# Kernel optimization log

Measured on AMD Instinct MI355X. Metric: run time of the kernel, lower is better.

Reference implementation:

```python
import jax, jax.numpy as jnp
import numpy as np
from jax import lax

D_MODEL = 2048
D_STATE = 16
D_CONV = 4
D_INNER = 4096   # expand * d_model
DT_RANK = 128    # ceil(d_model / 16)
BATCH = 4
SEQLEN = 2048


def setup_inputs() -> dict:
    key = jax.random.key(0)
    ks = jax.random.split(key, 8)
    rnd = lambda k, shape, s: jax.random.normal(k, shape, dtype=jnp.float32) * s
    hidden_states = rnd(ks[0], (BATCH, SEQLEN, D_MODEL), 1.0)
    in_proj_w = rnd(ks[1], (2 * D_INNER, D_MODEL), D_MODEL ** -0.5)
    conv_w = rnd(ks[2], (D_INNER, 1, D_CONV), 0.3)
    conv_b = rnd(ks[3], (D_INNER,), 0.1)
    x_proj_w = rnd(ks[4], (DT_RANK + 2 * D_STATE, D_INNER), D_INNER ** -0.5)
    dt_proj_w = rnd(ks[5], (D_INNER, DT_RANK), DT_RANK ** -0.5)
    dt_proj_b = rnd(ks[6], (D_INNER,), 0.5) - 2.0  # bias dt small, like mamba dt init
    out_proj_w = rnd(ks[7], (D_MODEL, D_INNER), D_INNER ** -0.5)
    # A init: -exp(log(arange(1..N))) broadcast over channels -> (d_state, d_inner)
    A = -jnp.tile(jnp.arange(1, D_STATE + 1, dtype=jnp.float32)[:, None], (1, D_INNER))
    D = jnp.ones((D_INNER,), dtype=jnp.float32)
    conv_state = jnp.zeros((BATCH, D_INNER, D_CONV), jnp.float32)
    ssm_state = jnp.zeros((BATCH, D_STATE, D_INNER), jnp.float32)
    last_token_ids = jnp.full((BATCH,), SEQLEN, dtype=jnp.int32)
    return dict(hidden_states=hidden_states, last_token_ids=last_token_ids,
                conv_state=conv_state, ssm_state=ssm_state,
                remove_padding=False, batch_size=BATCH,
                in_proj_w=in_proj_w, conv_w=conv_w, conv_b=conv_b,
                x_proj_w=x_proj_w, dt_proj_w=dt_proj_w, dt_proj_b=dt_proj_b,
                A=A, D=D, out_proj_w=out_proj_w)


def _mamba_forward(hidden_states, in_proj_w, conv_w, conv_b, x_proj_w,
                   dt_proj_w, dt_proj_b, A, D, out_proj_w):
    b, L, _ = hidden_states.shape
    # in_proj (no bias)
    xz = jnp.einsum('bld,ed->ble', hidden_states, in_proj_w)          # (b, L, 2*d_inner)
    x, z = jnp.split(xz, 2, axis=-1)
    x_bdl = x.transpose(0, 2, 1)                                       # (b, d_inner, L)
    # present conv state = last d_conv columns of pre-conv x (F.pad with negative pad)
    new_conv_state = x_bdl[:, :, L - D_CONV:]
    # causal depthwise conv1d (left pad d_conv-1 == pad-both then truncate to L)
    x_conv = lax.conv_general_dilated(
        x_bdl, conv_w, window_strides=(1,), padding=[(D_CONV - 1, 0)],
        feature_group_count=D_INNER,
        dimension_numbers=('NCH', 'OIH', 'NCH')) + conv_b[None, :, None]
    u = jax.nn.silu(x_conv).transpose(0, 2, 1)                          # (b, L, d_inner)
    # x_proj -> dt, B, C
    x_dbl = jnp.einsum('bld,ed->ble', u, x_proj_w)
    dt, Bm, Cm = jnp.split(x_dbl, [DT_RANK, DT_RANK + D_STATE], axis=-1)
    dt = jnp.einsum('blr,dr->bld', dt, dt_proj_w)                       # no bias here
    # selective scan (delta_bias=dt_proj_b, delta_softplus=True)
    delta = jax.nn.softplus(dt + dt_proj_b)                             # (b, L, d_inner)
    dBu = delta * u                                                     # (b, L, d_inner)

    def step(x_state, inp):
        d_i, bu_i, B_i, C_i = inp                                       # (b,d),(b,d),(b,n),(b,n)
        dA = jnp.exp(d_i[:, None, :] * A[None])                         # (b, n, d)
        x_state = dA * x_state + B_i[:, :, None] * bu_i[:, None, :]
        y = jnp.einsum('bnd,bn->bd', x_state, C_i)
        return x_state, y

    x0 = jnp.zeros((b, D_STATE, D_INNER), jnp.float32)
    xs = (delta.transpose(1, 0, 2), dBu.transpose(1, 0, 2),
          Bm.transpose(1, 0, 2), Cm.transpose(1, 0, 2))
    last_state, ys = lax.scan(step, x0, xs)
    y = ys.transpose(1, 0, 2) + u * D                                   # + D skip
    y = y * jax.nn.silu(z)                                              # gate
    out = jnp.einsum('bld,ed->ble', y, out_proj_w)                      # out_proj (no bias)
    return out, new_conv_state, last_state


def reference(hidden_states, last_token_ids, conv_state, ssm_state,
              remove_padding, batch_size,
              in_proj_w, conv_w, conv_b, x_proj_w, dt_proj_w, dt_proj_b,
              A, D, out_proj_w):
    # remove_padding=False and last_token_ids all == L: the torch per-sequence
    # loop is exactly one batched forward_impl with seqlen_offset=0.
    return _mamba_forward(hidden_states, in_proj_w, conv_w, conv_b, x_proj_w,
                          dt_proj_w, dt_proj_b, A, D, out_proj_w)
```

## Files before the change

kernel.cpp:

```cpp
#include <hip/hip_runtime.h>
#include <hip/hip_bf16.h>
#include <math.h>

typedef __attribute__((ext_vector_type(4))) float fvec4;
typedef __attribute__((ext_vector_type(2))) float fvec2;
typedef __attribute__((ext_vector_type(4))) int ivec4;
typedef __attribute__((ext_vector_type(4))) unsigned short usvec4;
typedef __attribute__((ext_vector_type(8))) short bf16x8;

#define SEQ 2048
#define DMODEL 2048
#define DINNER 4096
#define DSTATE 16
#define DTRANK 128
#define NB 4
#define MROWS (NB*SEQ)
#define NCHUNK 16
#define LC (SEQ/NCHUNK)

__device__ __forceinline__ float bf2f(unsigned short h){
  union{unsigned int u; float f;} v; v.u = ((unsigned int)h)<<16; return v.f;
}
__device__ __forceinline__ unsigned short f2bf(float f){
  union{float f; unsigned int u;} v; v.f=f;
  unsigned int r = v.u + 0x7fffu + ((v.u>>16)&1u);
  return (unsigned short)(r>>16);
}
__device__ __forceinline__ void async16(const void* g, void* l){
  __builtin_amdgcn_global_load_lds((const __attribute__((address_space(1))) void*)g,
                                   (__attribute__((address_space(3))) void*)l, 16, 0, 0);
}
__device__ __forceinline__ float sigf(float x){ return 1.f/(1.f+__expf(-x)); }

__global__ void cvt_bf16_kernel(const float* __restrict__ in, unsigned short* __restrict__ out, int n){
  int i = (blockIdx.x*256 + threadIdx.x)*4;
  if (i >= n) return;
  fvec4 v = *(const fvec4*)(in + i);
  usvec4 o;
  o[0]=f2bf(v[0]); o[1]=f2bf(v[1]); o[2]=f2bf(v[2]); o[3]=f2bf(v[3]);
  *(usvec4*)(out + i) = o;
}

template<int MODE>
__global__ __launch_bounds__(512, 2) void gemm256(
    const unsigned short* __restrict__ A,
    const unsigned short* __restrict__ B,
    int K, int nbx, int ldc,
    unsigned short* __restrict__ Cb1,
    unsigned short* __restrict__ Cb2,
    float* __restrict__ Cf)
{
  __shared__ __align__(16) unsigned short lds[65536];
  char* ldsc = (char*)lds;
  const int t = threadIdx.x;

  const int nwg = gridDim.x;
  const int cpx = nwg >> 3;
  const int bid = blockIdx.x;
  const int swzb = (bid & 7)*cpx + (bid >> 3);
  const int bx = swzb % nbx, by = swzb / nbx;

  const int bA0 = t*16, bA1 = 8192 + t*16;
  const int sw0 = bA0 ^ (((bA0>>7)&3)<<4);
  const int sw1 = bA1 ^ (((bA1>>7)&3)<<4);
  const int gr0 = sw0>>6, gc0 = (sw0&63)>>1;
  const int gr1 = sw1>>6, gc1 = (sw1&63)>>1;
  const unsigned short* Ab = A + (long)by*256*K;
  const unsigned short* Bb = B + (long)bx*256*K;
  const unsigned short* gA0 = Ab + (long)gr0*K + gc0;
  const unsigned short* gA1 = Ab + (long)gr1*K + gc1;
  const unsigned short* gB0 = Bb + (long)gr0*K + gc0;
  const unsigned short* gB1 = Bb + (long)gr1*K + gc1;

  const int wid = t>>6, lane = t&63;
  const int wm = wid>>2, wn = wid&3;
  const int fr = lane&15, fc = lane>>4;
  const int cb = (fc<<4) ^ (((fr>>1)&3)<<4);
  const int offA = (wm*128 + fr)*64 + cb;
  const int offB = 16384 + (wn*64 + fr)*64 + cb;

  fvec4 acc[8][4];
  #pragma unroll
  for (int i=0;i<8;i++){
    #pragma unroll
    for (int j=0;j<4;j++) acc[i][j] = (fvec4)(0.f);
  }

  const int NKT = K >> 5;
  auto stage = [&](int slot, int k0){
    char* sb = ldsc + slot*32768;
    async16(gA0 + k0, sb + t*16);
    async16(gA1 + k0, sb + 8192 + t*16);
    async16(gB0 + k0, sb + 16384 + t*16);
    async16(gB1 + k0, sb + 24576 + t*16);
  };

  stage(0, 0); stage(1, 32); stage(2, 64);

  for (int kt = 0; kt < NKT; ++kt){
    asm volatile("s_waitcnt vmcnt(8)" ::: "memory");
    __builtin_amdgcn_s_barrier();
    __builtin_amdgcn_sched_barrier(0);
    { int ks = kt + 3; if (ks > NKT-1) ks = NKT-1;
      stage((kt+3)&3, ks*32); }
    __builtin_amdgcn_sched_barrier(0);
    const char* sb = ldsc + (kt&3)*32768;
    bf16x8 af[8], bv[4];
    #pragma unroll
    for (int j=0;j<4;j++) bv[j] = *(const bf16x8*)(sb + offB + j*1024);
    #pragma unroll
    for (int i=0;i<8;i++) af[i] = *(const bf16x8*)(sb + offA + i*1024);
    __builtin_amdgcn_s_setprio(1);
    #pragma unroll
    for (int i=0;i<8;i++){
      #pragma unroll
      for (int j=0;j<4;j++){
        acc[i][j] = __builtin_amdgcn_mfma_f32_16x16x32_bf16(af[i], bv[j], acc[i][j], 0,0,0);
      }
    }
    __builtin_amdgcn_s_setprio(0);
  }

  const long crow0 = (long)by*256 + wm*128;
  const int  ccol0 = bx*256 + wn*64;
  #pragma unroll
  for (int i=0;i<8;i++){
    #pragma unroll
    for (int j=0;j<4;j++){
      #pragma unroll
      for (int q=0;q<4;q++){
        long rg = crow0 + i*16 + fc*4 + q;
        int  cg = ccol0 + j*16 + fr;
        float v = acc[i][j][q];
        if (MODE==0){
          if (cg < DINNER) Cb1[rg*DINNER + cg] = f2bf(v);
          else             Cb2[rg*DINNER + (cg-DINNER)] = f2bf(v);
        } else {
          Cf[rg*(long)ldc + cg] = v;
        }
      }
    }
  }
}

template<int MODE>
__global__ __launch_bounds__(256) void gemm_bt(
    const unsigned short* __restrict__ A,
    const unsigned short* __restrict__ B,
    int K, int Nreal,
    float* __restrict__ Cf,
    unsigned short* __restrict__ Cb1,
    const float* __restrict__ bias,
    int ldc)
{
  __shared__ __align__(16) unsigned short As[128*32];
  __shared__ __align__(16) unsigned short Bs[128*32];
  const int t = threadIdx.x;
  const int bx = blockIdx.x, by = blockIdx.y;
  const int wave = t>>6, lane = t&63;
  const int wr = (wave>>1)*64, wc = (wave&1)*64;
  const int fr = lane&15, fc = lane>>4;
  fvec4 acc[4][4];
  #pragma unroll
  for(int i=0;i<4;i++){
    #pragma unroll
    for(int j=0;j<4;j++){ acc[i][j] = (fvec4)(0.f); }
  }
  const int srow = t>>2;
  const int scol = (t&3)*8;
  long rowA = (long)by*128 + srow;
  int rB0 = bx*128 + srow;      if (rB0 > Nreal-1) rB0 = Nreal-1;
  int rB1 = bx*128 + 64 + srow; if (rB1 > Nreal-1) rB1 = Nreal-1;
  const unsigned short* gA0 = A + rowA*(long)K + scol;
  const unsigned short* gA1 = gA0 + 64L*K;
  const unsigned short* gB0 = B + (long)rB0*K + scol;
  const unsigned short* gB1 = B + (long)rB1*K + scol;
  unsigned short* lA0 = &As[t*8];
  unsigned short* lA1 = &As[2048 + t*8];
  unsigned short* lB0 = &Bs[t*8];
  unsigned short* lB1 = &Bs[2048 + t*8];

  for (int k0 = 0; k0 < K; k0 += 32){
    async16(gA0 + k0, lA0);
    async16(gA1 + k0, lA1);
    async16(gB0 + k0, lB0);
    async16(gB1 + k0, lB1);
    __syncthreads();
    bf16x8 af[4], bv[4];
    #pragma unroll
    for(int i=0;i<4;i++){
      af[i] = *(const bf16x8*)&As[(wr + i*16 + fr)*32 + fc*8];
      bv[i] = *(const bf16x8*)&Bs[(wc + i*16 + fr)*32 + fc*8];
    }
    #pragma unroll
    for(int i=0;i<4;i++){
      #pragma unroll
      for(int j=0;j<4;j++){
        acc[i][j] = __builtin_amdgcn_mfma_f32_16x16x32_bf16(af[i], bv[j], acc[i][j], 0,0,0);
      }
    }
    __syncthreads();
  }

  const long crow0 = (long)by*128 + wr;
  const int ccol0 = bx*128 + wc;
  #pragma unroll
  for(int i=0;i<4;i++){
    #pragma unroll
    for(int j=0;j<4;j++){
      #pragma unroll
      for(int q=0;q<4;q++){
        long rg = crow0 + i*16 + fc*4 + q;
        int  cg = ccol0 + j*16 + fr;
        float v = acc[i][j][q];
        if (MODE==1){
          if (cg < Nreal) Cf[rg*ldc + cg] = v;
        } else if (MODE==2){
          float x = v + bias[cg];
          float sp = (x > 20.f) ? x : log1pf(__expf(x));
          Cb1[rg*ldc + cg] = f2bf(sp);
        }
      }
    }
  }
}

__global__ __launch_bounds__(256) void conv_silu_kernel(
    const unsigned short* __restrict__ xb, const float* __restrict__ w,
    const float* __restrict__ bias, unsigned short* __restrict__ ub)
{
  int gid = blockIdx.x*256 + threadIdx.x;
  int d0 = (gid & 511)*8;
  long m = gid >> 9;
  int l = (int)(m & (SEQ-1));
  fvec4 w4[8];
  #pragma unroll
  for(int k=0;k<8;k++) w4[k] = *(const fvec4*)&w[(d0+k)*4];
  float acc[8];
  fvec4 b0 = *(const fvec4*)&bias[d0];
  fvec4 b1 = *(const fvec4*)&bias[d0+4];
  acc[0]=b0[0];acc[1]=b0[1];acc[2]=b0[2];acc[3]=b0[3];
  acc[4]=b1[0];acc[5]=b1[1];acc[6]=b1[2];acc[7]=b1[3];
  #pragma unroll
  for(int j=0;j<4;j++){
    int lj = l-3+j;
    if (lj >= 0){
      ivec4 xv = *(const ivec4*)&xb[(m-3+j)*DINNER + d0];
      float xs[8];
      #pragma unroll
      for(int q=0;q<4;q++){
        unsigned int wd = (unsigned int)xv[q];
        xs[2*q]   = bf2f((unsigned short)(wd & 0xffffu));
        xs[2*q+1] = bf2f((unsigned short)(wd >> 16));
      }
      #pragma unroll
      for(int k=0;k<8;k++) acc[k] += xs[k]*w4[k][j];
    }
  }
  ivec4 ov;
  #pragma unroll
  for(int q=0;q<4;q++){
    float y0 = acc[2*q]  * sigf(acc[2*q]);
    float y1 = acc[2*q+1]* sigf(acc[2*q+1]);
    ov[q] = (int)((unsigned)f2bf(y0) | ((unsigned)f2bf(y1) << 16));
  }
  *(ivec4*)&ub[m*DINNER + d0] = ov;
}

__global__ void conv_state_kernel(const unsigned short* __restrict__ xb, float* __restrict__ out){
  int i = blockIdx.x*256 + threadIdx.x;
  int b = i >> 14; int r = i & 16383; int dd = r >> 2; int j = r & 3;
  out[i] = bf2f(xb[((long)(b*SEQ + (SEQ-4) + j))*DINNER + dd]);
}

__global__ void cvt_dtr_kernel(const float* __restrict__ xdbl, unsigned short* __restrict__ dtr){
  int i = blockIdx.x*256 + threadIdx.x;
  long mrow = i >> 5; int c = (i & 31)*4;
  fvec4 v = *(const fvec4*)&xdbl[mrow*160 + c];
  usvec4 o; o[0]=f2bf(v[0]); o[1]=f2bf(v[1]); o[2]=f2bf(v[2]); o[3]=f2bf(v[3]);
  *(usvec4*)&dtr[mrow*DTRANK + c] = o;
}

__device__ __forceinline__ void exp_powers(float dl, float* e){
  float e1 = __expf(-dl);
  float p2 = e1*e1, p3 = p2*e1, p4 = p2*p2;
  float p5 = p4*e1, p6 = p4*p2, p7 = p4*p3, p8 = p4*p4;
  e[0]=e1; e[1]=p2; e[2]=p3; e[3]=p4; e[4]=p5; e[5]=p6; e[6]=p7; e[7]=p8;
  e[8]=p8*e1; e[9]=p8*p2; e[10]=p8*p3; e[11]=p8*p4;
  e[12]=p8*p5; e[13]=p8*p6; e[14]=p8*p7; e[15]=p8*p8;
}

__global__ __launch_bounds__(256) void scan_part1(
    const unsigned short* __restrict__ delta_b,
    const unsigned short* __restrict__ u_b,
    const float* __restrict__ xdbl,
    const float* __restrict__ Amat,
    float* __restrict__ S,
    float* __restrict__ sdelta)
{
  const int t = threadIdx.x;
  const int blk = blockIdx.x;
  const int c = blk & 15, b = (blk>>4)&3, d = (blk>>6)*256 + t;
  float a[16], s[16];
  #pragma unroll
  for (int n=0;n<16;n++){ a[n] = Amat[n*DINNER+d]; s[n]=0.f; }
  bool powA = true;
  #pragma unroll
  for (int n=0;n<16;n++) powA = powA && (a[n] == -(float)(n+1));
  float sd = 0.f;
  const long mbase = (long)b*SEQ + c*LC;

#define S1_BODY(EXPR_E) \
  for (int l=0;l<LC;l++){ \
    long m = mbase + l; \
    float dl = bf2f(delta_b[m*DINNER+d]); \
    float ul = bf2f(u_b[m*DINNER+d]); \
    const float* xb = &xdbl[m*160 + 128]; \
    float dbu = dl*ul; \
    sd += dl; \
    float e[16]; EXPR_E; \
    _Pragma("unroll") \
    for (int g=0; g<4; g++){ \
      fvec4 Bg = *(const fvec4*)(xb + 4*g); \
      _Pragma("unroll") \
      for (int q=0;q<4;q++){ \
        int n = g*4+q; \
        s[n] = e[n]*s[n] + Bg[q]*dbu; \
      } \
    } \
  }

  if (powA){
    S1_BODY(exp_powers(dl, e))
  } else {
    S1_BODY({ _Pragma("unroll") for (int n=0;n<16;n++) e[n] = __expf(dl*a[n]); })
  }
#undef S1_BODY

  const long base = ((long)(b*NCHUNK + c)*DSTATE)*DINNER + d;
  #pragma unroll
  for (int n=0;n<16;n++) S[base + (long)n*DINNER] = s[n];
  sdelta[(long)(b*NCHUNK+c)*DINNER + d] = sd;
}

__global__ __launch_bounds__(256) void scan_part2(
    const float* __restrict__ S,
    const float* __restrict__ sdelta,
    const float* __restrict__ Amat,
    float* __restrict__ Xin,
    float* __restrict__ last_state)
{
  int id = blockIdx.x*256 + threadIdx.x;
  int d = id & (DINNER-1);
  int n = (id>>12) & 15;
  int b = id>>16;
  float a = Amat[n*DINNER+d];
  float X = 0.f;
  #pragma unroll
  for (int c=0;c<NCHUNK;c++){
    long sb = ((long)(b*NCHUNK+c)*DSTATE + n)*DINNER + d;
    Xin[sb] = X;
    float sd = sdelta[(long)(b*NCHUNK+c)*DINNER + d];
    float Sc = S[sb];
    X = __expf(a*sd)*X + Sc;
  }
  last_state[((long)b*DSTATE + n)*DINNER + d] = X;
}

__global__ __launch_bounds__(256) void scan_part3(
    const unsigned short* __restrict__ delta_b,
    const unsigned short* __restrict__ u_b,
    const unsigned short* __restrict__ z_b,
    const float* __restrict__ xdbl,
    const float* __restrict__ Amat,
    const float* __restrict__ Dvec,
    const float* __restrict__ Xin,
    unsigned short* __restrict__ y_b)
{
  const int t = threadIdx.x;
  const int blk = blockIdx.x;
  const int c = blk & 15, b = (blk>>4)&3, d = (blk>>6)*256 + t;
  float a[16], s[16];
  const long xb0 = ((long)(b*NCHUNK + c)*DSTATE)*DINNER + d;
  #pragma unroll
  for (int n=0;n<16;n++){
    a[n] = Amat[n*DINNER+d];
    s[n] = Xin[xb0 + (long)n*DINNER];
  }
  bool powA = true;
  #pragma unroll
  for (int n=0;n<16;n++) powA = powA && (a[n] == -(float)(n+1));
  const float Dd = Dvec[d];
  const long mbase = (long)b*SEQ + c*LC;

#define S3_BODY(EXPR_E) \
  for (int l=0;l<LC;l++){ \
    long m = mbase + l; \
    float dl = bf2f(delta_b[m*DINNER+d]); \
    float ul = bf2f(u_b[m*DINNER+d]); \
    float zl = bf2f(z_b[m*DINNER+d]); \
    const float* xb = &xdbl[m*160 + 128]; \
    float dbu = dl*ul; \
    float y = 0.f; \
    float e[16]; EXPR_E; \
    _Pragma("unroll") \
    for (int g=0; g<4; g++){ \
      fvec4 Bg = *(const fvec4*)(xb + 4*g); \
      fvec4 Cg = *(const fvec4*)(xb + 16 + 4*g); \
      _Pragma("unroll") \
      for (int q=0;q<4;q++){ \
        int n = g*4+q; \
        s[n] = e[n]*s[n] + Bg[q]*dbu; \
        y += Cg[q]*s[n]; \
      } \
    } \
    float yy = y + ul*Dd; \
    float zs = zl*sigf(zl); \
    y_b[m*DINNER+d] = f2bf(yy*zs); \
  }

  if (powA){
    S3_BODY(exp_powers(dl, e))
  } else {
    S3_BODY({ _Pragma("unroll") for (int n=0;n<16;n++) e[n] = __expf(dl*a[n]); })
  }
#undef S3_BODY
}

extern "C" void kernel_launch(void* const* d_in, const int* in_sizes, int n_in,
                              void* d_out, int out_size, void* d_ws, size_t ws_size,
                              hipStream_t stream) {
  const float* hs     = (const float*)d_in[0];
  const float* w_in   = (const float*)d_in[6];
  const float* conv_w = (const float*)d_in[7];
  const float* conv_b = (const float*)d_in[8];
  const float* w_xp   = (const float*)d_in[9];
  const float* w_dt   = (const float*)d_in[10];
  const float* dt_bias= (const float*)d_in[11];
  const float* Amat   = (const float*)d_in[12];
  const float* Dvec   = (const float*)d_in[13];
  const float* w_out  = (const float*)d_in[14];
  float* out = (float*)d_out;

  char* ws = (char*)d_ws;
  const size_t MiB = (size_t)1 << 20;

  unsigned short *hs_b, *w_in_b, *x_b, *z_b, *u_b, *delta_b;
  unsigned short *wxp_b, *wdt_b, *wout_b, *dtr_b, *y_b;
  float *xdbl, *Sbuf, *Xin, *sdelta;

  if (ws_size >= 400*MiB){
    size_t off = 0;
    auto alloc = [&](size_t bytes)->void*{ void* p = ws + off; off += (bytes + 255) & ~(size_t)255; return p; };
    hs_b   = (unsigned short*)alloc((size_t)MROWS*DMODEL*2);
    w_in_b = (unsigned short*)alloc((size_t)2*DINNER*DMODEL*2);
    x_b    = (unsigned short*)alloc((size_t)MROWS*DINNER*2);
    z_b    = (unsigned short*)alloc((size_t)MROWS*DINNER*2);
    u_b    = (unsigned short*)alloc((size_t)MROWS*DINNER*2);
    delta_b= (unsigned short*)alloc((size_t)MROWS*DINNER*2);
    wxp_b  = (unsigned short*)alloc((size_t)160*DINNER*2);
    wdt_b  = (unsigned short*)alloc((size_t)DINNER*DTRANK*2);
    wout_b = (unsigned short*)alloc((size_t)DMODEL*DINNER*2);
    xdbl   = (float*)alloc((size_t)MROWS*160*4);
    dtr_b  = (unsigned short*)alloc((size_t)MROWS*DTRANK*2);
    Sbuf   = (float*)alloc((size_t)NB*NCHUNK*DSTATE*DINNER*4);
    Xin    = (float*)alloc((size_t)NB*NCHUNK*DSTATE*DINNER*4);
    sdelta = (float*)alloc((size_t)NB*NCHUNK*DINNER*4);
    y_b    = x_b;
  } else {
    hs_b    = (unsigned short*)(ws + 0);
    w_in_b  = (unsigned short*)(ws + 32*MiB);
    delta_b = (unsigned short*)(ws + 0);
    x_b     = (unsigned short*)(ws + 64*MiB);
    wxp_b   = (unsigned short*)(ws + 64*MiB);
    wdt_b   = (unsigned short*)(ws + 66*MiB);
    wout_b  = (unsigned short*)(ws + 68*MiB);
    xdbl    = (float*)         (ws + 84*MiB);
    dtr_b   = (unsigned short*)(ws + 90*MiB);
    Sbuf    = (float*)         (ws + 92*MiB);
    Xin     = (float*)         (ws + 108*MiB);
    sdelta  = (float*)         (ws + 124*MiB);
    z_b     = (unsigned short*)(ws + 128*MiB);
    u_b     = (unsigned short*)(ws + 192*MiB);
    y_b     = u_b;
  }

  cvt_bf16_kernel<<<(MROWS*DMODEL)/1024, 256, 0, stream>>>(hs, hs_b, MROWS*DMODEL);
  cvt_bf16_kernel<<<(2*DINNER*DMODEL)/1024, 256, 0, stream>>>(w_in, w_in_b, 2*DINNER*DMODEL);

  gemm256<0><<<1024, 512, 0, stream>>>(hs_b, w_in_b, DMODEL, 32, 0,
                                       x_b, z_b, nullptr);
  conv_state_kernel<<<256, 256, 0, stream>>>(x_b, out + (size_t)MROWS*DMODEL);
  conv_silu_kernel<<<(MROWS*512)/256, 256, 0, stream>>>(x_b, conv_w, conv_b, u_b);

  cvt_bf16_kernel<<<(160*DINNER)/1024, 256, 0, stream>>>(w_xp, wxp_b, 160*DINNER);
  cvt_bf16_kernel<<<(DINNER*DTRANK)/1024, 256, 0, stream>>>(w_dt, wdt_b, DINNER*DTRANK);
  cvt_bf16_kernel<<<(DMODEL*DINNER)/1024, 256, 0, stream>>>(w_out, wout_b, DMODEL*DINNER);

  gemm_bt<1><<<dim3(2,64), 256, 0, stream>>>(u_b, wxp_b, DINNER, 160,
                                             xdbl, nullptr, nullptr, 160);
  cvt_dtr_kernel<<<(MROWS*32)/256, 256, 0, stream>>>(xdbl, dtr_b);
  gemm_bt<2><<<dim3(32,64), 256, 0, stream>>>(dtr_b, wdt_b, DTRANK, DINNER,
                                              nullptr, delta_b, dt_bias, DINNER);
  scan_part1<<<1024, 256, 0, stream>>>(delta_b, u_b, xdbl, Amat, Sbuf, sdelta);
  scan_part2<<<1024, 256, 0, stream>>>(Sbuf, sdelta, Amat, Xin,
                                       out + (size_t)MROWS*DMODEL + NB*DINNER*4);
  scan_part3<<<1024, 256, 0, stream>>>(delta_b, u_b, z_b, xdbl, Amat, Dvec, Xin, y_b);
  gemm256<3><<<256, 512, 0, stream>>>(y_b, wout_b, DINNER, 8, DMODEL,
                                      nullptr, nullptr, out);
}
```

Baseline: 912.5 us.

## Split-K the x_proj GEMM and software-pipeline LDS fragment loads in gemm256

The x_proj GEMM (N=160, K=4096) ran on only 128 blocks. It now splits K four ways across blockIdx.z into partial buffers. A new reduce kernel sums the partials and also emits the bf16 dt_rank slice, replacing cvt_dtr_kernel. Separately, the 256x256 GEMM main loop is reorganised into half-steps that prefetch the next stage's A/B fragments from LDS while MFMAs run on the current ones, with a looser vmcnt wait. This adds partial-buffer traffic and workspace, and raises register pressure in the big GEMM.

```diff
diff --git a/kernel.cpp b/kernel.cpp
--- a/kernel.cpp
+++ b/kernel.cpp
@@ -97,29 +97,52 @@
 
   stage(0, 0); stage(1, 32); stage(2, 64);
 
-  for (int kt = 0; kt < NKT; ++kt){
-    asm volatile("s_waitcnt vmcnt(8)" ::: "memory");
-    __builtin_amdgcn_s_barrier();
-    __builtin_amdgcn_sched_barrier(0);
-    { int ks = kt + 3; if (ks > NKT-1) ks = NKT-1;
-      stage((kt+3)&3, ks*32); }
-    __builtin_amdgcn_sched_barrier(0);
-    const char* sb = ldsc + (kt&3)*32768;
-    bf16x8 af[8], bv[4];
-    #pragma unroll
-    for (int j=0;j<4;j++) bv[j] = *(const bf16x8*)(sb + offB + j*1024);
-    #pragma unroll
-    for (int i=0;i<8;i++) af[i] = *(const bf16x8*)(sb + offA + i*1024);
-    __builtin_amdgcn_s_setprio(1);
-    #pragma unroll
-    for (int i=0;i<8;i++){
-      #pragma unroll
-      for (int j=0;j<4;j++){
-        acc[i][j] = __builtin_amdgcn_mfma_f32_16x16x32_bf16(af[i], bv[j], acc[i][j], 0,0,0);
-      }
-    }
-    __builtin_amdgcn_s_setprio(0);
-  }
+  bf16x8 aP[4], aQ[4], bU[4], bV[4];
+  asm volatile("s_waitcnt vmcnt(8)" ::: "memory");
+  __builtin_amdgcn_s_barrier();
+  __builtin_amdgcn_sched_barrier(0);
+  #pragma unroll
+  for (int i=0;i<4;i++) aP[i] = *(const bf16x8*)(ldsc + offA + i*1024);
+  #pragma unroll
+  for (int j=0;j<4;j++) bU[j] = *(const bf16x8*)(ldsc + offB + j*1024);
+
+#define GEM_HALF(KT, BC, BN) { \
+    const char* cs = ldsc + ((KT)&3)*32768; \
+    const char* ns = ldsc + (((KT)+1)&3)*32768; \
+    asm volatile("s_waitcnt vmcnt(4)" ::: "memory"); \
+    __builtin_amdgcn_s_barrier(); \
+    __builtin_amdgcn_sched_barrier(0); \
+    { int ks = (KT) + 3; if (ks > NKT-1) ks = NKT-1; stage(((KT)+3)&3, ks*32); } \
+    __builtin_amdgcn_sched_barrier(0); \
+    _Pragma("unroll") \
+    for (int i=0;i<4;i++) aQ[i] = *(const bf16x8*)(cs + offA + (4+i)*1024); \
+    __builtin_amdgcn_s_setprio(1); \
+    _Pragma("unroll") \
+    for (int i=0;i<4;i++){ \
+      _Pragma("unroll") \
+      for (int j=0;j<4;j++) \
+        acc[i][j] = __builtin_amdgcn_mfma_f32_16x16x32_bf16(aP[i], BC[j], acc[i][j], 0,0,0); \
+    } \
+    __builtin_amdgcn_s_setprio(0); \
+    _Pragma("unroll") \
+    for (int i=0;i<4;i++) aP[i] = *(const bf16x8*)(ns + offA + i*1024); \
+    _Pragma("unroll") \
+    for (int j=0;j<4;j++) BN[j] = *(const bf16x8*)(ns + offB + j*1024); \
+    __builtin_amdgcn_s_setprio(1); \
+    _Pragma("unroll") \
+    for (int i=0;i<4;i++){ \
+      _Pragma("unroll") \
+      for (int j=0;j<4;j++) \
+        acc[4+i][j] = __builtin_amdgcn_mfma_f32_16x16x32_bf16(aQ[i], BC[j], acc[4+i][j], 0,0,0); \
+    } \
+    __builtin_amdgcn_s_setprio(0); \
+  }
+
+  for (int kt = 0; kt < NKT; kt += 2){
+    GEM_HALF(kt,   bU, bV);
+    GEM_HALF(kt+1, bV, bU);
+  }
+#undef GEM_HALF
 
   const long crow0 = (long)by*256 + wm*128;
   const int  ccol0 = bx*256 + wn*64;
@@ -147,7 +170,7 @@
 __global__ __launch_bounds__(256) void gemm_bt(
     const unsigned short* __restrict__ A,
     const unsigned short* __restrict__ B,
-    int K, int Nreal,
+    int lda, int Kloop, int Nreal,
     float* __restrict__ Cf,
     unsigned short* __restrict__ Cb1,
     const float* __restrict__ bias,
@@ -157,6 +180,7 @@
   __shared__ __align__(16) unsigned short Bs[128*32];
   const int t = threadIdx.x;
   const int bx = blockIdx.x, by = blockIdx.y;
+  const long koff = (MODE==4) ? (long)blockIdx.z * Kloop : 0;
   const int wave = t>>6, lane = t&63;
   const int wr = (wave>>1)*64, wc = (wave&1)*64;
   const int fr = lane&15, fc = lane>>4;
@@ -171,16 +195,16 @@
   long rowA = (long)by*128 + srow;
   int rB0 = bx*128 + srow;      if (rB0 > Nreal-1) rB0 = Nreal-1;
   int rB1 = bx*128 + 64 + srow; if (rB1 > Nreal-1) rB1 = Nreal-1;
-  const unsigned short* gA0 = A + rowA*(long)K + scol;
-  const unsigned short* gA1 = gA0 + 64L*K;
-  const unsigned short* gB0 = B + (long)rB0*K + scol;
-  const unsigned short* gB1 = B + (long)rB1*K + scol;
+  const unsigned short* gA0 = A + rowA*(long)lda + scol + koff;
+  const unsigned short* gA1 = gA0 + 64L*lda;
+  const unsigned short* gB0 = B + (long)rB0*lda + scol + koff;
+  const unsigned short* gB1 = B + (long)rB1*lda + scol + koff;
   unsigned short* lA0 = &As[t*8];
   unsigned short* lA1 = &As[2048 + t*8];
   unsigned short* lB0 = &Bs[t*8];
   unsigned short* lB1 = &Bs[2048 + t*8];
 
-  for (int k0 = 0; k0 < K; k0 += 32){
+  for (int k0 = 0; k0 < Kloop; k0 += 32){
     async16(gA0 + k0, lA0);
     async16(gA1 + k0, lA1);
     async16(gB0 + k0, lB0);
@@ -204,6 +228,7 @@
 
   const long crow0 = (long)by*128 + wr;
   const int ccol0 = bx*128 + wc;
+  float* Cfz = (MODE==4) ? (Cf + (long)blockIdx.z * MROWS * ldc) : Cf;
   #pragma unroll
   for(int i=0;i<4;i++){
     #pragma unroll
@@ -213,8 +238,8 @@
         long rg = crow0 + i*16 + fc*4 + q;
         int  cg = ccol0 + j*16 + fr;
         float v = acc[i][j][q];
-        if (MODE==1){
-          if (cg < Nreal) Cf[rg*ldc + cg] = v;
+        if (MODE==4){
+          if (cg < Nreal) Cfz[rg*ldc + cg] = v;
         } else if (MODE==2){
           float x = v + bias[cg];
           float sp = (x > 20.f) ? x : log1pf(__expf(x));
@@ -222,6 +247,26 @@
         }
       }
     }
+  }
+}
+
+__global__ void reduce_xproj(const float* __restrict__ part,
+                             float* __restrict__ xdbl,
+                             unsigned short* __restrict__ dtr){
+  int i = blockIdx.x*256 + threadIdx.x;
+  long base = (long)i*4;
+  fvec4 s = *(const fvec4*)&part[base];
+  #pragma unroll
+  for (int z=1; z<4; z++){
+    fvec4 p = *(const fvec4*)&part[(long)z*MROWS*160 + base];
+    s[0]+=p[0]; s[1]+=p[1]; s[2]+=p[2]; s[3]+=p[3];
+  }
+  *(fvec4*)&xdbl[base] = s;
+  long mrow = base / 160;
+  int c = (int)(base - mrow*160);
+  if (c < DTRANK){
+    usvec4 o; o[0]=f2bf(s[0]); o[1]=f2bf(s[1]); o[2]=f2bf(s[2]); o[3]=f2bf(s[3]);
+    *(usvec4*)&dtr[mrow*DTRANK + c] = o;
   }
 }
 
@@ -271,14 +316,6 @@
   int i = blockIdx.x*256 + threadIdx.x;
   int b = i >> 14; int r = i & 16383; int dd = r >> 2; int j = r & 3;
   out[i] = bf2f(xb[((long)(b*SEQ + (SEQ-4) + j))*DINNER + dd]);
-}
-
-__global__ void cvt_dtr_kernel(const float* __restrict__ xdbl, unsigned short* __restrict__ dtr){
-  int i = blockIdx.x*256 + threadIdx.x;
-  long mrow = i >> 5; int c = (i & 31)*4;
-  fvec4 v = *(const fvec4*)&xdbl[mrow*160 + c];
-  usvec4 o; o[0]=f2bf(v[0]); o[1]=f2bf(v[1]); o[2]=f2bf(v[2]); o[3]=f2bf(v[3]);
-  *(usvec4*)&dtr[mrow*DTRANK + c] = o;
 }
 
 __device__ __forceinline__ void exp_powers(float dl, float* e){
@@ -447,9 +484,9 @@
 
   unsigned short *hs_b, *w_in_b, *x_b, *z_b, *u_b, *delta_b;
   unsigned short *wxp_b, *wdt_b, *wout_b, *dtr_b, *y_b;
-  float *xdbl, *Sbuf, *Xin, *sdelta;
-
-  if (ws_size >= 400*MiB){
+  float *xdbl, *Sbuf, *Xin, *sdelta, *xpart;
+
+  if (ws_size >= 424*MiB){
     size_t off = 0;
     auto alloc = [&](size_t bytes)->void*{ void* p = ws + off; off += (bytes + 255) & ~(size_t)255; return p; };
     hs_b   = (unsigned short*)alloc((size_t)MROWS*DMODEL*2);
@@ -466,10 +503,12 @@
     Sbuf   = (float*)alloc((size_t)NB*NCHUNK*DSTATE*DINNER*4);
     Xin    = (float*)alloc((size_t)NB*NCHUNK*DSTATE*DINNER*4);
     sdelta = (float*)alloc((size_t)NB*NCHUNK*DINNER*4);
+    xpart  = (float*)alloc((size_t)4*MROWS*160*4);
     y_b    = x_b;
   } else {
     hs_b    = (unsigned short*)(ws + 0);
     w_in_b  = (unsigned short*)(ws + 32*MiB);
+    xpart   = (float*)         (ws + 0);
     delta_b = (unsigned short*)(ws + 0);
     x_b     = (unsigned short*)(ws + 64*MiB);
     wxp_b   = (unsigned short*)(ws + 64*MiB);
@@ -497,10 +536,10 @@
   cvt_bf16_kernel<<<(DINNER*DTRANK)/1024, 256, 0, stream>>>(w_dt, wdt_b, DINNER*DTRANK);
   cvt_bf16_kernel<<<(DMODEL*DINNER)/1024, 256, 0, stream>>>(w_out, wout_b, DMODEL*DINNER);
 
-  gemm_bt<1><<<dim3(2,64), 256, 0, stream>>>(u_b, wxp_b, DINNER, 160,
-                                             xdbl, nullptr, nullptr, 160);
-  cvt_dtr_kernel<<<(MROWS*32)/256, 256, 0, stream>>>(xdbl, dtr_b);
-  gemm_bt<2><<<dim3(32,64), 256, 0, stream>>>(dtr_b, wdt_b, DTRANK, DINNER,
+  gemm_bt<4><<<dim3(2,64,4), 256, 0, stream>>>(u_b, wxp_b, DINNER, 1024, 160,
+                                               xpart, nullptr, nullptr, 160);
+  reduce_xproj<<<(MROWS*160/4)/256, 256, 0, stream>>>(xpart, xdbl, dtr_b);
+  gemm_bt<2><<<dim3(32,64), 256, 0, stream>>>(dtr_b, wdt_b, DTRANK, DTRANK, DINNER,
                                               nullptr, delta_b, dt_bias, DINNER);
   scan_part1<<<1024, 256, 0, stream>>>(delta_b, u_b, xdbl, Amat, Sbuf, sdelta);
   scan_part2<<<1024, 256, 0, stream>>>(Sbuf, sdelta, Amat, Xin,
```

After: 856.7 us. 6.1% less time.
